# Performance work log

Hardware: AMD Instinct MI355X
Metric: run time of the kernel (lower is better)

The kernel has to match this reference:

```python
import jax, jax.numpy as jnp
import numpy as np

EPS = 1e-5


def setup_inputs() -> dict:
    key = jax.random.key(0)
    ks = jax.random.split(key, 7)
    BATCH, nbr, L, K, U = 64, 16, 64, 32, 4
    in1, in2, out = 64, 8, 32  # in2 = 2*U, out = K

    def unif(k, shape, fan_out, fan_in):
        ini = float(np.sqrt(3.0 / fan_out / fan_in))
        return jax.random.uniform(k, shape, jnp.float32, -ini, ini)

    return {
        "Hhat_real": jax.random.normal(ks[0], (BATCH, nbr, L, K, U), jnp.float32),
        "Hhat_imag": jax.random.normal(ks[1], (BATCH, nbr, L, K, U), jnp.float32),
        "Vhat": jax.random.normal(ks[2], (BATCH, nbr, L, K, U), jnp.float32),
        "Qs_hidden": unif(ks[3], (2, 4, in1, in1), in1, in1),  # Q1_AP,Q2_AP,Q1_UE,Q2_UE per hidden layer
        "Ps_hidden": unif(ks[4], (2, 2, in1, in2), in1, in2),  # P1_AP,P1_UE per hidden layer
        "Qs_out": unif(ks[5], (4, out, in1), out, in1),
        "Ps_out": unif(ks[6], (2, out, in2), out, in2),
        "bn_gamma": jnp.ones((2, in1), jnp.float32),
        "bn_beta": jnp.zeros((2, in1), jnp.float32),
        "nbrOfRealizations": nbr,
        "L": L,
        "K": K,
        "U": U,
    }


def _bn(x, gamma, beta):
    # BatchNorm1d in training mode: per-channel stats over (batch, spatial), biased variance
    m = x.mean(axis=(0, 2), keepdims=True)
    v = x.var(axis=(0, 2), keepdims=True)
    return (x - m) / jnp.sqrt(v + EPS) * gamma[None, :, None] + beta[None, :, None]


def _layer(A_AP, A_UE, H, Q1a, Q2a, Q1u, Q2u, P1a, P1u, gamma, beta, act):
    # A_AP: [B, in1, L], A_UE: [B, in1, K], H: [B, in2, L, K]
    new_AP = (2.0 * jnp.einsum('oi,bil->bol', Q1a, A_AP)
              + 2.0 * jnp.einsum('oi,bi->bo', Q2a, A_UE.mean(-1))[:, :, None]
              + 0.1 * jnp.einsum('oi,bil->bol', P1a, H.mean(-1)))
    new_UE = (2.0 * jnp.einsum('oi,bik->bok', Q1u, A_UE)
              + 2.0 * jnp.einsum('oi,bi->bo', Q2u, A_AP.mean(-1))[:, :, None]
              + 0.1 * jnp.einsum('oi,bik->bok', P1u, H.mean(-2)))
    if act:
        new_AP = jax.nn.relu(new_AP)
        new_UE = jax.nn.relu(new_UE)
    if gamma is not None:
        new_AP = _bn(new_AP, gamma, beta)
        new_UE = _bn(new_UE, gamma, beta)
    return new_AP, new_UE


def _forward(Hhat_real, Hhat_imag, Vhat, Qs_hidden, Ps_hidden, Qs_out, Ps_out,
             bn_gamma, bn_beta, nbr, L, K, U):
    BATCH = Hhat_real.shape[0]
    B = BATCH * nbr
    in1 = Qs_hidden.shape[-1]
    # [B,1,L,K,U] -> transpose(2,3) -> transpose(2,4) == permute (0,1,4,2,3)
    Hr = jnp.transpose(Hhat_real.reshape(B, 1, L, K, U), (0, 1, 4, 2, 3))
    Hi = jnp.transpose(Hhat_imag.reshape(B, 1, L, K, U), (0, 1, 4, 2, 3))
    H = jnp.concatenate([Hr, Hi], axis=1).reshape(B, 2 * U, L, K)  # [B, 2U, L, K]

    A_AP = jnp.zeros((B, in1, L), H.dtype)
    A_UE = jnp.zeros((B, in1, K), H.dtype)
    n_hidden = Qs_hidden.shape[0]
    for i in range(n_hidden):
        A_AP, A_UE = _layer(A_AP, A_UE, H,
                            Qs_hidden[i, 0], Qs_hidden[i, 1], Qs_hidden[i, 2], Qs_hidden[i, 3],
                            Ps_hidden[i, 0], Ps_hidden[i, 1],
                            bn_gamma[i], bn_beta[i], act=True)
    V_AP_out, _ = _layer(A_AP, A_UE, H,
                         Qs_out[0], Qs_out[1], Qs_out[2], Qs_out[3],
                         Ps_out[0], Ps_out[1], None, None, act=False)  # [B, K, L]

    Phat1 = jnp.swapaxes(V_AP_out.reshape(BATCH, nbr, K, L), 2, 3)  # [BATCH, nbr, L, K]
    norm = jnp.linalg.norm(Phat1, axis=2, keepdims=True)            # [BATCH, nbr, 1, K]
    Phat = Phat1 / norm * np.sqrt(float(L))
    Fhat = Vhat.reshape(BATCH, nbr, L, K, U) * Phat[..., None]
    return Fhat


def reference(Hhat_real, Hhat_imag, Vhat, Qs_hidden, Ps_hidden, Qs_out, Ps_out,
              bn_gamma, bn_beta, nbrOfRealizations, L, K, U):
    return _forward(Hhat_real, Hhat_imag, Vhat, Qs_hidden, Ps_hidden, Qs_out, Ps_out,
                    bn_gamma, bn_beta, int(nbrOfRealizations), int(L), int(K), int(U))
```

## Files before the change

kernel.cpp:

```cpp
#include <hip/hip_runtime.h>

#define B_TOT 1024
#define L_DIM 64
#define K_DIM 32
#define OUT_K 32
#define EPS_BN 1e-5f

typedef __attribute__((ext_vector_type(8))) short short8;
typedef __attribute__((ext_vector_type(4))) float f32x4;

__device__ __forceinline__ float reduce64(float v) {
    #pragma unroll
    for (int w = 1; w < 64; w <<= 1) v += __shfl_xor(v, w);
    return v;
}

template<int CTRL, int RM>
__device__ __forceinline__ float dppadd(float v) {
    return v + __int_as_float(__builtin_amdgcn_update_dpp(
        0, __float_as_int(v), CTRL, RM, 0xF, true));
}
__device__ __forceinline__ float sum64_dpp(float v) {
    v = dppadd<0x111, 0xF>(v);
    v = dppadd<0x112, 0xF>(v);
    v = dppadd<0x114, 0xF>(v);
    v = dppadd<0x118, 0xF>(v);
    v = dppadd<0x142, 0xA>(v);
    v = dppadd<0x143, 0xC>(v);
    return v;
}
__device__ __forceinline__ float sum32_dpp(float v) {
    v = dppadd<0x111, 0xF>(v);
    v = dppadd<0x112, 0xF>(v);
    v = dppadd<0x114, 0xF>(v);
    v = dppadd<0x118, 0xF>(v);
    v = dppadd<0x142, 0xA>(v);
    return v;
}

__device__ __forceinline__ unsigned short f2bf(float x) {
    unsigned int u = __float_as_uint(x);
    u += 0x7FFF + ((u >> 16) & 1);
    return (unsigned short)(u >> 16);
}

__global__ __launch_bounds__(256, 4) void hmeans_l0_kernel(
    const float* __restrict__ Hr, const float* __restrict__ Hi,
    float* __restrict__ Hmk, float* __restrict__ Hml,
    const float* __restrict__ P0,
    float* __restrict__ muS, float* __restrict__ muQ,
    const float* __restrict__ Qh1,
    const float* __restrict__ P1h,
    const float* __restrict__ Qo,
    float* __restrict__ QTo,
    unsigned short* __restrict__ Qpack_ap,
    unsigned short* __restrict__ Qpack_ue) {
    int b = blockIdx.x, tid = threadIdx.x;

    if (b == B_TOT) {
        for (int idx = tid; idx < 2048; idx += 256) {
            int i = idx >> 5, o = idx & 31;
            QTo[idx] = Qo[o * 64 + i];
        }
        const float* Q1a = Qh1;
        const float* Q1u = Qh1 + 2 * 4096;
        const float* P1a = P1h;
        const float* P1u = P1h + 512;
        for (int idx = tid; idx < 6144; idx += 256) {
            int j = idx & 7, lane = (idx >> 3) & 63, ot = (idx >> 9) & 3, kt = idx >> 11;
            int m = lane & 15, kloc = (lane >> 4) * 8 + j;
            int o = ot * 16 + m, k = kt * 32 + kloc;
            float va = 0.f, vu = 0.f;
            if (k < 64)      { va = 2.0f * Q1a[o * 64 + k]; vu = 2.0f * Q1u[o * 64 + k]; }
            else if (k < 72) { va = 0.1f * P1a[o * 8 + (k - 64)]; vu = 0.1f * P1u[o * 8 + (k - 64)]; }
            Qpack_ap[idx] = f2bf(va);
            Qpack_ue[idx] = f2bf(vu);
        }
        return;
    }

    __shared__ float hmkS[512];
    __shared__ float hmlS[256];
    __shared__ float4 wpart[4][32];
    int w = tid >> 6, lane = tid & 63;
    int g = tid >> 5, k = tid & 31;

    for (int ri = 0; ri < 2; ++ri) {
        const float4* src4 = (const float4*)((ri ? Hi : Hr) + (size_t)b * 8192);
        float4 v[8];
        #pragma unroll
        for (int s = 0; s < 8; ++s) v[s] = src4[tid + 256 * s];

        float4 part = v[0];
        #pragma unroll
        for (int s = 1; s < 8; ++s) {
            part.x += v[s].x; part.y += v[s].y;
            part.z += v[s].z; part.w += v[s].w;
        }

        #pragma unroll
        for (int s = 0; s < 8; ++s) {
            float rx = sum32_dpp(v[s].x);
            float ry = sum32_dpp(v[s].y);
            float rz = sum32_dpp(v[s].z);
            float rw = sum32_dpp(v[s].w);
            if ((lane & 31) == 31) {
                int l = g + 8 * s;
                const float sc = 1.0f / 32.0f;
                hmkS[(ri * 4 + 0) * 64 + l] = rx * sc;
                hmkS[(ri * 4 + 1) * 64 + l] = ry * sc;
                hmkS[(ri * 4 + 2) * 64 + l] = rz * sc;
                hmkS[(ri * 4 + 3) * 64 + l] = rw * sc;
            }
        }

        part.x += __shfl_xor(part.x, 32);
        part.y += __shfl_xor(part.y, 32);
        part.z += __shfl_xor(part.z, 32);
        part.w += __shfl_xor(part.w, 32);
        if (lane < 32) wpart[w][k] = part;
        __syncthreads();
        if (tid < 128) {
            int kk = tid >> 2, u = tid & 3;
            float s = ((const float*)&wpart[0][kk])[u]
                    + ((const float*)&wpart[1][kk])[u]
                    + ((const float*)&wpart[2][kk])[u]
                    + ((const float*)&wpart[3][kk])[u];
            hmlS[(ri * 4 + u) * 32 + kk] = s * (1.0f / 64.0f);
        }
        __syncthreads();
    }

    Hmk[(size_t)b * 512 + tid]       = hmkS[tid];
    Hmk[(size_t)b * 512 + 256 + tid] = hmkS[256 + tid];
    Hml[(size_t)b * 256 + tid]       = hmlS[tid];

    int o0 = __builtin_amdgcn_readfirstlane(w << 4);
    float hmk[8], hml[8];
    #pragma unroll
    for (int c = 0; c < 8; ++c) hmk[c] = hmkS[c * 64 + lane];
    #pragma unroll
    for (int c = 0; c < 8; ++c) hml[c] = hmlS[c * 32 + (lane & 31)];

    for (int h = 0; h < 2; ++h) {
        float vs[8], qs[8];
        #pragma unroll
        for (int mm = 0; mm < 8; ++mm) {
            int o = o0 + h * 8 + mm;
            float4 p0 = *(const float4*)(P0 + o * 8);
            float4 p1 = *(const float4*)(P0 + o * 8 + 4);
            float pa = p0.x * hmk[0] + p0.y * hmk[1] + p0.z * hmk[2] + p0.w * hmk[3]
                     + p1.x * hmk[4] + p1.y * hmk[5] + p1.z * hmk[6] + p1.w * hmk[7];
            float v = fmaxf(0.1f * pa, 0.f);
            vs[mm] = sum64_dpp(v);
            qs[mm] = sum64_dpp(v * v);
        }
        if (lane == 63) {
            #pragma unroll
            for (int mm = 0; mm < 8; ++mm) {
                muS[b * 128 + o0 + h * 8 + mm] = vs[mm];
                muQ[b * 128 + o0 + h * 8 + mm] = qs[mm];
            }
        }
    }
    for (int h = 0; h < 2; ++h) {
        float vs[8], qs[8];
        #pragma unroll
        for (int mm = 0; mm < 8; ++mm) {
            int o = o0 + h * 8 + mm;
            float4 p0 = *(const float4*)(P0 + 512 + o * 8);
            float4 p1 = *(const float4*)(P0 + 512 + o * 8 + 4);
            float pu = p0.x * hml[0] + p0.y * hml[1] + p0.z * hml[2] + p0.w * hml[3]
                     + p1.x * hml[4] + p1.y * hml[5] + p1.z * hml[6] + p1.w * hml[7];
            float v = fmaxf(0.1f * pu, 0.f);
            vs[mm] = sum64_dpp(v);
            qs[mm] = sum64_dpp(v * v);
        }
        if (lane == 63) {
            #pragma unroll
            for (int mm = 0; mm < 8; ++mm) {
                muS[b * 128 + 64 + o0 + h * 8 + mm] = vs[mm] * 0.5f;
                muQ[b * 128 + 64 + o0 + h * 8 + mm] = qs[mm] * 0.5f;
            }
        }
    }
}

__global__ __launch_bounds__(256, 2) void layer_hidden1_kernel(
    float* __restrict__ Aap_out,
    const float* __restrict__ Hmk, const float* __restrict__ Hml,
    const unsigned short* __restrict__ Qpack_ap,
    const unsigned short* __restrict__ Qpack_ue,
    const float* __restrict__ P0,
    const float* __restrict__ coefA,
    const float* __restrict__ biasIn,
    float* __restrict__ muS, float* __restrict__ muQ) {
    __shared__ unsigned short Bap[64 * 104];
    __shared__ unsigned short Bue[32 * 104];
    int b = blockIdx.x, t = threadIdx.x;

    {
        int l = t & 63, wid = t >> 6, i0 = wid << 4;
        float hmk[8];
        #pragma unroll
        for (int c = 0; c < 8; ++c) hmk[c] = Hmk[(size_t)b * 512 + c * 64 + l];
        unsigned short tmp[16];
        #pragma unroll
        for (int m = 0; m < 16; ++m) {
            int i = i0 + m;
            float4 p0 = *(const float4*)(P0 + i * 8);
            float4 p1 = *(const float4*)(P0 + i * 8 + 4);
            float pa = p0.x * hmk[0] + p0.y * hmk[1] + p0.z * hmk[2] + p0.w * hmk[3]
                     + p1.x * hmk[4] + p1.y * hmk[5] + p1.z * hmk[6] + p1.w * hmk[7];
            float a0 = fmaxf(0.1f * pa, 0.f);
            tmp[m] = f2bf(a0 * coefA[i] + coefA[64 + i]);
        }
        short8 s0, s1;
        #pragma unroll
        for (int j = 0; j < 8; ++j) { s0[j] = (short)tmp[j]; s1[j] = (short)tmp[8 + j]; }
        *(short8*)(&Bap[l * 104 + i0]) = s0;
        *(short8*)(&Bap[l * 104 + i0 + 8]) = s1;
        if (wid == 0) {
            #pragma unroll
            for (int c = 0; c < 8; ++c) Bap[l * 104 + 64 + c] = f2bf(hmk[c]);
            #pragma unroll
            for (int c = 72; c < 96; ++c) Bap[l * 104 + c] = 0;
        }
    }
    {
        int k = t & 31, g = t >> 5, i0 = g << 3;
        float hml[8];
        #pragma unroll
        for (int c = 0; c < 8; ++c) hml[c] = Hml[(size_t)b * 256 + c * 32 + k];
        unsigned short tu[8];
        #pragma unroll
        for (int m = 0; m < 8; ++m) {
            int i = i0 + m;
            float4 p0 = *(const float4*)(P0 + 512 + i * 8);
            float4 p1 = *(const float4*)(P0 + 512 + i * 8 + 4);
            float pu = p0.x * hml[0] + p0.y * hml[1] + p0.z * hml[2] + p0.w * hml[3]
                     + p1.x * hml[4] + p1.y * hml[5] + p1.z * hml[6] + p1.w * hml[7];
            float a0 = fmaxf(0.1f * pu, 0.f);
            tu[m] = f2bf(a0 * coefA[128 + i] + coefA[192 + i]);
        }
        short8 s0;
        #pragma unroll
        for (int j = 0; j < 8; ++j) s0[j] = (short)tu[j];
        *(short8*)(&Bue[k * 104 + i0]) = s0;
        if (t < 32) {
            #pragma unroll
            for (int c = 0; c < 8; ++c) Bue[k * 104 + 64 + c] = f2bf(hml[c]);
            #pragma unroll
            for (int c = 72; c < 96; ++c) Bue[k * 104 + c] = 0;
        }
    }
    __syncthreads();

    int lane = t & 63, w = t >> 6;
    int m16 = lane & 15, g4 = lane >> 4;
    int obase = w * 16 + g4 * 4;

    short8 aq[3], aqu[3];
    #pragma unroll
    for (int kt = 0; kt < 3; ++kt) {
        aq[kt]  = *(const short8*)(Qpack_ap + (((kt * 4 + w) * 64 + lane) << 3));
        aqu[kt] = *(const short8*)(Qpack_ue + (((kt * 4 + w) * 64 + lane) << 3));
    }

    float vsum[4] = {0.f, 0.f, 0.f, 0.f}, vsq[4] = {0.f, 0.f, 0.f, 0.f};
    #pragma unroll
    for (int lt = 0; lt < 4; ++lt) {
        f32x4 acc = *(const f32x4*)(biasIn + b * 128 + obase);
        #pragma unroll
        for (int kt = 0; kt < 3; ++kt) {
            short8 bf = *(const short8*)(&Bap[(lt * 16 + m16) * 104 + kt * 32 + g4 * 8]);
            acc = __builtin_amdgcn_mfma_f32_16x16x32_bf16(aq[kt], bf, acc, 0, 0, 0);
        }
        int lsp = lt * 16 + m16;
        #pragma unroll
        for (int r = 0; r < 4; ++r) {
            float v = fmaxf(acc[r], 0.f);
            Aap_out[(size_t)b * 4096 + (obase + r) * 64 + lsp] = v;
            vsum[r] += v; vsq[r] += v * v;
        }
    }
    #pragma unroll
    for (int s = 1; s < 16; s <<= 1) {
        #pragma unroll
        for (int r = 0; r < 4; ++r) {
            vsum[r] += __shfl_xor(vsum[r], s);
            vsq[r]  += __shfl_xor(vsq[r], s);
        }
    }
    if (m16 == 0) {
        #pragma unroll
        for (int r = 0; r < 4; ++r) {
            muS[b * 128 + obase + r] = vsum[r];
            muQ[b * 128 + obase + r] = vsq[r];
        }
    }

    float usum[4] = {0.f, 0.f, 0.f, 0.f}, usq[4] = {0.f, 0.f, 0.f, 0.f};
    #pragma unroll
    for (int nt = 0; nt < 2; ++nt) {
        f32x4 acc = *(const f32x4*)(biasIn + b * 128 + 64 + obase);
        #pragma unroll
        for (int kt = 0; kt < 3; ++kt) {
            short8 bf = *(const short8*)(&Bue[(nt * 16 + m16) * 104 + kt * 32 + g4 * 8]);
            acc = __builtin_amdgcn_mfma_f32_16x16x32_bf16(aqu[kt], bf, acc, 0, 0, 0);
        }
        #pragma unroll
        for (int r = 0; r < 4; ++r) {
            float v = fmaxf(acc[r], 0.f);
            usum[r] += v; usq[r] += v * v;
        }
    }
    #pragma unroll
    for (int s = 1; s < 16; s <<= 1) {
        #pragma unroll
        for (int r = 0; r < 4; ++r) {
            usum[r] += __shfl_xor(usum[r], s);
            usq[r]  += __shfl_xor(usq[r], s);
        }
    }
    if (m16 == 0) {
        #pragma unroll
        for (int r = 0; r < 4; ++r) {
            muS[b * 128 + 64 + obase + r] = usum[r];
            muQ[b * 128 + 64 + obase + r] = usq[r];
        }
    }
}

__global__ __launch_bounds__(256, 8) void bn_finalize_kernel(
    const float* __restrict__ muS, const float* __restrict__ muQ,
    const float* __restrict__ gamma, const float* __restrict__ beta,
    float* __restrict__ coef) {
    __shared__ float redS[4], redQ[4];
    int ch = blockIdx.x;
    int tid = threadIdx.x;
    float s = 0.f, q = 0.f;
    for (int j = tid; j < 1024; j += 256) {
        s += muS[j * 128 + ch];
        q += muQ[j * 128 + ch];
    }
    s = reduce64(s);
    q = reduce64(q);
    int wave = tid >> 6, lane = tid & 63;
    if (lane == 0) { redS[wave] = s; redQ[wave] = q; }
    __syncthreads();
    if (tid == 0) {
        s = redS[0] + redS[1] + redS[2] + redS[3];
        q = redQ[0] + redQ[1] + redQ[2] + redQ[3];
        bool ap = ch < 64;
        int o = ap ? ch : ch - 64;
        float cnt = ap ? (float)(B_TOT * L_DIM) : (float)(B_TOT * K_DIM);
        float m = s / cnt;
        float var = q / cnt - m * m;
        float sc = gamma[o] / sqrtf(var + EPS_BN);
        if (ap) { coef[o] = sc;       coef[64 + o] = beta[o] - m * sc; }
        else    { coef[128 + o] = sc; coef[192 + o] = beta[o] - m * sc; }
    }
}

__global__ __launch_bounds__(128, 8) void bias_hidden_kernel(
    const float* __restrict__ Q, const float* __restrict__ coef,
    const float* __restrict__ muS, float* __restrict__ bias) {
    __shared__ float mubn[128];
    int b = blockIdx.x, t = threadIdx.x;
    float raw = muS[b * 128 + t];
    if (t < 64) mubn[t] = raw * (1.0f / 64.0f) * coef[t] + coef[64 + t];
    else        mubn[t] = raw * (1.0f / 32.0f) * coef[64 + t] + coef[128 + t];
    __syncthreads();
    const float* Qm = (t < 64) ? (Q + 4096) : (Q + 3 * 4096);
    const float* mu = (t < 64) ? (mubn + 64) : mubn;
    int o = t & 63;
    const float4* Qrow = (const float4*)(Qm + o * 64);
    float sa = 0.f, sb = 0.f, sc2 = 0.f, sd = 0.f;
    #pragma unroll
    for (int j = 0; j < 16; ++j) {
        float4 q = Qrow[j];
        sa += q.x * mu[4 * j];
        sb += q.y * mu[4 * j + 1];
        sc2 += q.z * mu[4 * j + 2];
        sd += q.w * mu[4 * j + 3];
    }
    bias[b * 128 + t] = 2.f * ((sa + sb) + (sc2 + sd));
}

__global__ __launch_bounds__(64, 8) void bias_out_kernel(
    const float* __restrict__ Qo, const float* __restrict__ coef,
    const float* __restrict__ muS, float* __restrict__ biasO) {
    __shared__ float mubn[64];
    int b = blockIdx.x, t = threadIdx.x;
    mubn[t] = muS[b * 128 + 64 + t] * (1.0f / 32.0f) * coef[128 + t] + coef[192 + t];
    __syncthreads();
    if (t < 32) {
        const float4* Qrow = (const float4*)(Qo + OUT_K * 64 + t * 64);
        float sa = 0.f, sb = 0.f, sc2 = 0.f, sd = 0.f;
        #pragma unroll
        for (int j = 0; j < 16; ++j) {
            float4 q = Qrow[j];
            sa += q.x * mubn[4 * j];
            sb += q.y * mubn[4 * j + 1];
            sc2 += q.z * mubn[4 * j + 2];
            sd += q.w * mubn[4 * j + 3];
        }
        biasO[b * 32 + t] = 2.f * ((sa + sb) + (sc2 + sd));
    }
}

__global__ __launch_bounds__(256, 4) void layer_out_fin_kernel(
    const float* __restrict__ Aap_in,
    const float* __restrict__ Hmk,
    const float* __restrict__ QTo,
    const float* __restrict__ Po,
    const float* __restrict__ coefIn,
    const float* __restrict__ biasO,
    const float* __restrict__ Vhat,
    float* __restrict__ out) {
    __shared__ float sV[32 * 65];
    __shared__ float inv[32];
    int b = blockIdx.x, tid = threadIdx.x;
    int wid = tid >> 6, lane = tid & 63;
    int ob = __builtin_amdgcn_readfirstlane(wid << 3);

    float hmk[8];
    #pragma unroll
    for (int c = 0; c < 8; ++c) hmk[c] = Hmk[(size_t)b * 512 + c * 64 + lane];

    float bp[8];
    #pragma unroll
    for (int m = 0; m < 8; ++m) {
        int o = ob + m;
        float4 p0 = *(const float4*)(Po + o * 8);
        float4 p1 = *(const float4*)(Po + o * 8 + 4);
        float pa = p0.x * hmk[0] + p0.y * hmk[1] + p0.z * hmk[2] + p0.w * hmk[3]
                 + p1.x * hmk[4] + p1.y * hmk[5] + p1.z * hmk[6] + p1.w * hmk[7];
        bp[m] = 0.1f * pa + biasO[b * 32 + o];
    }

    float acc[8];
    #pragma unroll
    for (int m = 0; m < 8; ++m) acc[m] = 0.f;
    {
        const float* A_in = Aap_in + (size_t)b * 4096 + lane;
        #pragma unroll 4
        for (int i = 0; i < 64; ++i) {
            float x = A_in[i * 64];
            float aa = x * coefIn[i] + coefIn[64 + i];
            float4 q0 = *(const float4*)(QTo + i * 32 + ob);
            float4 q1 = *(const float4*)(QTo + i * 32 + ob + 4);
            acc[0] += q0.x * aa; acc[1] += q0.y * aa;
            acc[2] += q0.z * aa; acc[3] += q0.w * aa;
            acc[4] += q1.x * aa; acc[5] += q1.y * aa;
            acc[6] += q1.z * aa; acc[7] += q1.w * aa;
        }
    }
    #pragma unroll
    for (int m = 0; m < 8; ++m)
        sV[(ob + m) * 65 + lane] = 2.f * acc[m] + bp[m];

    __syncthreads();
    if (tid < 32) {
        float s = 0.f;
        #pragma unroll
        for (int l = 0; l < 64; ++l) { float x = sV[tid * 65 + l]; s += x * x; }
        inv[tid] = 8.0f / sqrtf(s);
    }
    __syncthreads();
    const float4* vh4 = (const float4*)(Vhat + (size_t)b * 8192);
    float4* o4 = (float4*)out + (size_t)b * 2048;
    for (int j = tid; j < 2048; j += 256) {
        int l = j >> 5, kk = j & 31;
        float p = sV[kk * 65 + l] * inv[kk];
        float4 x = vh4[j];
        x.x *= p; x.y *= p; x.z *= p; x.w *= p;
        o4[j] = x;
    }
}

extern "C" void kernel_launch(void* const* d_in, const int* in_sizes, int n_in,
                              void* d_out, int out_size, void* d_ws, size_t ws_size,
                              hipStream_t stream) {
    const float* Hr        = (const float*)d_in[0];
    const float* Hi        = (const float*)d_in[1];
    const float* Vhat      = (const float*)d_in[2];
    const float* Qs_hidden = (const float*)d_in[3];
    const float* Ps_hidden = (const float*)d_in[4];
    const float* Qs_out    = (const float*)d_in[5];
    const float* Ps_out    = (const float*)d_in[6];
    const float* bn_gamma  = (const float*)d_in[7];
    const float* bn_beta   = (const float*)d_in[8];
    float* out = (float*)d_out;

    float* ws    = (float*)d_ws;
    float* Hmk   = ws;
    float* Hml   = Hmk + 524288;
    float* AapB  = Hml + 262144;
    float* muS   = AapB + 4194304;
    float* muQ   = muS + 131072;
    float* coefA = muQ + 131072;
    float* coefB = coefA + 256;
    float* biasA = coefB + 256;
    float* biasO = biasA + 131072;
    float* QTo   = biasO + 32768;
    unsigned short* Qpack_ap = (unsigned short*)(QTo + 2048);
    unsigned short* Qpack_ue = Qpack_ap + 6144;

    hipLaunchKernelGGL(hmeans_l0_kernel, dim3(B_TOT + 1), dim3(256), 0, stream,
                       Hr, Hi, Hmk, Hml, Ps_hidden, muS, muQ,
                       Qs_hidden + 4 * 4096, Ps_hidden + 2 * 512, Qs_out,
                       QTo, Qpack_ap, Qpack_ue);
    hipLaunchKernelGGL(bn_finalize_kernel, dim3(128), dim3(256), 0, stream,
                       muS, muQ, bn_gamma, bn_beta, coefA);
    hipLaunchKernelGGL(bias_hidden_kernel, dim3(B_TOT), dim3(128), 0, stream,
                       Qs_hidden + 4 * 4096, coefA, muS, biasA);

    hipLaunchKernelGGL(layer_hidden1_kernel, dim3(B_TOT), dim3(256), 0, stream,
                       AapB, Hmk, Hml, Qpack_ap, Qpack_ue,
                       Ps_hidden, coefA, biasA, muS, muQ);
    hipLaunchKernelGGL(bn_finalize_kernel, dim3(128), dim3(256), 0, stream,
                       muS, muQ, bn_gamma + 64, bn_beta + 64, coefB);
    hipLaunchKernelGGL(bias_out_kernel, dim3(B_TOT), dim3(64), 0, stream,
                       Qs_out, coefB, muS, biasO);

    hipLaunchKernelGGL(layer_out_fin_kernel, dim3(B_TOT), dim3(256), 0, stream,
                       AapB, Hmk, QTo, Ps_out, coefB, biasO, Vhat, out);
}
```

Before: 77.18 us.

## Recompute layer-1 activations in output kernel instead of storing to global

```diff
diff --git a/kernel.cpp b/kernel.cpp
--- a/kernel.cpp
+++ b/kernel.cpp
@@ -7,6 +7,7 @@
 #define EPS_BN 1e-5f
 
 typedef __attribute__((ext_vector_type(8))) short short8;
+typedef __attribute__((ext_vector_type(4))) short short4v;
 typedef __attribute__((ext_vector_type(4))) float f32x4;
 
 __device__ __forceinline__ float reduce64(float v) {
@@ -37,6 +38,13 @@
     v = dppadd<0x142, 0xA>(v);
     return v;
 }
+__device__ __forceinline__ float sum16_dpp(float v) {
+    v = dppadd<0x111, 0xF>(v);
+    v = dppadd<0x112, 0xF>(v);
+    v = dppadd<0x114, 0xF>(v);
+    v = dppadd<0x118, 0xF>(v);
+    return v;
+}
 
 __device__ __forceinline__ unsigned short f2bf(float x) {
     unsigned int u = __float_as_uint(x);
@@ -52,16 +60,13 @@
     const float* __restrict__ Qh1,
     const float* __restrict__ P1h,
     const float* __restrict__ Qo,
-    float* __restrict__ QTo,
+    const float* __restrict__ Po,
     unsigned short* __restrict__ Qpack_ap,
-    unsigned short* __restrict__ Qpack_ue) {
+    unsigned short* __restrict__ Qpack_ue,
+    unsigned short* __restrict__ Qpack_o) {
     int b = blockIdx.x, tid = threadIdx.x;
 
     if (b == B_TOT) {
-        for (int idx = tid; idx < 2048; idx += 256) {
-            int i = idx >> 5, o = idx & 31;
-            QTo[idx] = Qo[o * 64 + i];
-        }
         const float* Q1a = Qh1;
         const float* Q1u = Qh1 + 2 * 4096;
         const float* P1a = P1h;
@@ -76,6 +81,15 @@
             Qpack_ap[idx] = f2bf(va);
             Qpack_ue[idx] = f2bf(vu);
         }
+        for (int idx = tid; idx < 3072; idx += 256) {
+            int j = idx & 7, lane = (idx >> 3) & 63, ot = (idx >> 9) & 1, kt = idx >> 10;
+            int m = lane & 15, kloc = (lane >> 4) * 8 + j;
+            int o = ot * 16 + m, k = kt * 32 + kloc;
+            float v = 0.f;
+            if (k < 64)      v = 2.0f * Qo[o * 64 + k];
+            else if (k < 72) v = 0.1f * Po[o * 8 + (k - 64)];
+            Qpack_o[idx] = f2bf(v);
+        }
         return;
     }
 
@@ -186,17 +200,19 @@
     }
 }
 
-__global__ __launch_bounds__(256, 2) void layer_hidden1_kernel(
-    float* __restrict__ Aap_out,
+__global__ __launch_bounds__(256, 2) void l1stats_kernel(
     const float* __restrict__ Hmk, const float* __restrict__ Hml,
     const unsigned short* __restrict__ Qpack_ap,
     const unsigned short* __restrict__ Qpack_ue,
     const float* __restrict__ P0,
+    const float* __restrict__ Qh1,
     const float* __restrict__ coefA,
-    const float* __restrict__ biasIn,
-    float* __restrict__ muS, float* __restrict__ muQ) {
+    const float* __restrict__ muS0,
+    float* __restrict__ muS1, float* __restrict__ muQ1) {
     __shared__ unsigned short Bap[64 * 104];
     __shared__ unsigned short Bue[32 * 104];
+    __shared__ float mubn[128];
+    __shared__ float biasS[128];
     int b = blockIdx.x, t = threadIdx.x;
 
     {
@@ -254,6 +270,30 @@
             for (int c = 72; c < 96; ++c) Bue[k * 104 + c] = 0;
         }
     }
+    if (t < 128) {
+        float raw = muS0[b * 128 + t];
+        mubn[t] = (t < 64)
+            ? raw * (1.0f / 64.0f) * coefA[t] + coefA[64 + t]
+            : raw * (1.0f / 32.0f) * coefA[64 + t] + coefA[128 + t];
+    }
+    __syncthreads();
+
+    if (t < 128) {
+        const float* Qm = (t < 64) ? (Qh1 + 4096) : (Qh1 + 3 * 4096);
+        const float* mu = (t < 64) ? (mubn + 64) : mubn;
+        int o = t & 63;
+        const float4* Qrow = (const float4*)(Qm + o * 64);
+        float sa = 0.f, sb = 0.f, sc2 = 0.f, sd = 0.f;
+        #pragma unroll
+        for (int j = 0; j < 16; ++j) {
+            float4 q = Qrow[j];
+            sa += q.x * mu[4 * j];
+            sb += q.y * mu[4 * j + 1];
+            sc2 += q.z * mu[4 * j + 2];
+            sd += q.w * mu[4 * j + 3];
+        }
+        biasS[t] = 2.f * ((sa + sb) + (sc2 + sd));
+    }
     __syncthreads();
 
     int lane = t & 63, w = t >> 6;
@@ -270,40 +310,35 @@
     float vsum[4] = {0.f, 0.f, 0.f, 0.f}, vsq[4] = {0.f, 0.f, 0.f, 0.f};
     #pragma unroll
     for (int lt = 0; lt < 4; ++lt) {
-        f32x4 acc = *(const f32x4*)(biasIn + b * 128 + obase);
+        f32x4 acc = *(const f32x4*)(&biasS[obase]);
         #pragma unroll
         for (int kt = 0; kt < 3; ++kt) {
             short8 bf = *(const short8*)(&Bap[(lt * 16 + m16) * 104 + kt * 32 + g4 * 8]);
             acc = __builtin_amdgcn_mfma_f32_16x16x32_bf16(aq[kt], bf, acc, 0, 0, 0);
         }
-        int lsp = lt * 16 + m16;
         #pragma unroll
         for (int r = 0; r < 4; ++r) {
             float v = fmaxf(acc[r], 0.f);
-            Aap_out[(size_t)b * 4096 + (obase + r) * 64 + lsp] = v;
             vsum[r] += v; vsq[r] += v * v;
         }
     }
     #pragma unroll
-    for (int s = 1; s < 16; s <<= 1) {
+    for (int r = 0; r < 4; ++r) {
+        vsum[r] = sum16_dpp(vsum[r]);
+        vsq[r]  = sum16_dpp(vsq[r]);
+    }
+    if (m16 == 15) {
         #pragma unroll
         for (int r = 0; r < 4; ++r) {
-            vsum[r] += __shfl_xor(vsum[r], s);
-            vsq[r]  += __shfl_xor(vsq[r], s);
-        }
-    }
-    if (m16 == 0) {
-        #pragma unroll
-        for (int r = 0; r < 4; ++r) {
-            muS[b * 128 + obase + r] = vsum[r];
-            muQ[b * 128 + obase + r] = vsq[r];
+            muS1[b * 128 + obase + r] = vsum[r];
+            muQ1[b * 128 + obase + r] = vsq[r];
         }
     }
 
     float usum[4] = {0.f, 0.f, 0.f, 0.f}, usq[4] = {0.f, 0.f, 0.f, 0.f};
     #pragma unroll
     for (int nt = 0; nt < 2; ++nt) {
-        f32x4 acc = *(const f32x4*)(biasIn + b * 128 + 64 + obase);
+        f32x4 acc = *(const f32x4*)(&biasS[64 + obase]);
         #pragma unroll
         for (int kt = 0; kt < 3; ++kt) {
             short8 bf = *(const short8*)(&Bue[(nt * 16 + m16) * 104 + kt * 32 + g4 * 8]);
@@ -316,18 +351,15 @@
         }
     }
     #pragma unroll
-    for (int s = 1; s < 16; s <<= 1) {
+    for (int r = 0; r < 4; ++r) {
+        usum[r] = sum16_dpp(usum[r]);
+        usq[r]  = sum16_dpp(usq[r]);
+    }
+    if (m16 == 15) {
         #pragma unroll
         for (int r = 0; r < 4; ++r) {
-            usum[r] += __shfl_xor(usum[r], s);
-            usq[r]  += __shfl_xor(usq[r], s);
-        }
-    }
-    if (m16 == 0) {
-        #pragma unroll
-        for (int r = 0; r < 4; ++r) {
-            muS[b * 128 + 64 + obase + r] = usum[r];
-            muQ[b * 128 + 64 + obase + r] = usq[r];
+            muS1[b * 128 + 64 + obase + r] = usum[r];
+            muQ1[b * 128 + 64 + obase + r] = usq[r];
         }
     }
 }
@@ -363,115 +395,163 @@
     }
 }
 
-__global__ __launch_bounds__(128, 8) void bias_hidden_kernel(
-    const float* __restrict__ Q, const float* __restrict__ coef,
-    const float* __restrict__ muS, float* __restrict__ bias) {
-    __shared__ float mubn[128];
+__global__ __launch_bounds__(256, 2) void out_fin_kernel(
+    const float* __restrict__ Hmk,
+    const unsigned short* __restrict__ Qpack_ap,
+    const unsigned short* __restrict__ Qpack_o,
+    const float* __restrict__ P0,
+    const float* __restrict__ Qh1,
+    const float* __restrict__ Qo,
+    const float* __restrict__ coefA,
+    const float* __restrict__ coefB,
+    const float* __restrict__ muS0,
+    const float* __restrict__ muS1,
+    const float* __restrict__ Vhat,
+    float* __restrict__ out) {
+    __shared__ unsigned short Bap[64 * 104];
+    __shared__ unsigned short B2[64 * 104];
+    __shared__ float sV[32 * 65];
+    __shared__ float mubnA[64], mubnB[64];
+    __shared__ float biasA_S[64], biasO_S[32];
+    __shared__ float cB[128];
+    __shared__ float inv[32];
     int b = blockIdx.x, t = threadIdx.x;
-    float raw = muS[b * 128 + t];
-    if (t < 64) mubn[t] = raw * (1.0f / 64.0f) * coef[t] + coef[64 + t];
-    else        mubn[t] = raw * (1.0f / 32.0f) * coef[64 + t] + coef[128 + t];
-    __syncthreads();
-    const float* Qm = (t < 64) ? (Q + 4096) : (Q + 3 * 4096);
-    const float* mu = (t < 64) ? (mubn + 64) : mubn;
-    int o = t & 63;
-    const float4* Qrow = (const float4*)(Qm + o * 64);
-    float sa = 0.f, sb = 0.f, sc2 = 0.f, sd = 0.f;
-    #pragma unroll
-    for (int j = 0; j < 16; ++j) {
-        float4 q = Qrow[j];
-        sa += q.x * mu[4 * j];
-        sb += q.y * mu[4 * j + 1];
-        sc2 += q.z * mu[4 * j + 2];
-        sd += q.w * mu[4 * j + 3];
-    }
-    bias[b * 128 + t] = 2.f * ((sa + sb) + (sc2 + sd));
-}
-
-__global__ __launch_bounds__(64, 8) void bias_out_kernel(
-    const float* __restrict__ Qo, const float* __restrict__ coef,
-    const float* __restrict__ muS, float* __restrict__ biasO) {
-    __shared__ float mubn[64];
-    int b = blockIdx.x, t = threadIdx.x;
-    mubn[t] = muS[b * 128 + 64 + t] * (1.0f / 32.0f) * coef[128 + t] + coef[192 + t];
-    __syncthreads();
-    if (t < 32) {
-        const float4* Qrow = (const float4*)(Qo + OUT_K * 64 + t * 64);
+    int lane = t & 63, w = t >> 6;
+
+    {
+        int l = lane, i0 = w << 4;
+        float hmk[8];
+        #pragma unroll
+        for (int c = 0; c < 8; ++c) hmk[c] = Hmk[(size_t)b * 512 + c * 64 + l];
+        unsigned short tmp[16];
+        #pragma unroll
+        for (int m = 0; m < 16; ++m) {
+            int i = i0 + m;
+            float4 p0 = *(const float4*)(P0 + i * 8);
+            float4 p1 = *(const float4*)(P0 + i * 8 + 4);
+            float pa = p0.x * hmk[0] + p0.y * hmk[1] + p0.z * hmk[2] + p0.w * hmk[3]
+                     + p1.x * hmk[4] + p1.y * hmk[5] + p1.z * hmk[6] + p1.w * hmk[7];
+            float a0 = fmaxf(0.1f * pa, 0.f);
+            tmp[m] = f2bf(a0 * coefA[i] + coefA[64 + i]);
+        }
+        short8 s0, s1;
+        #pragma unroll
+        for (int j = 0; j < 8; ++j) { s0[j] = (short)tmp[j]; s1[j] = (short)tmp[8 + j]; }
+        *(short8*)(&Bap[l * 104 + i0]) = s0;
+        *(short8*)(&Bap[l * 104 + i0 + 8]) = s1;
+        if (w == 0) {
+            #pragma unroll
+            for (int c = 0; c < 8; ++c) {
+                unsigned short hb = f2bf(hmk[c]);
+                Bap[l * 104 + 64 + c] = hb;
+                B2[l * 104 + 64 + c]  = hb;
+            }
+            #pragma unroll
+            for (int c = 72; c < 96; ++c) { Bap[l * 104 + c] = 0; B2[l * 104 + c] = 0; }
+        }
+    }
+    if (t < 64)  mubnA[t] = muS0[b * 128 + 64 + t] * (1.0f / 32.0f) * coefA[128 + t] + coefA[192 + t];
+    else if (t < 128) {
+        int i = t - 64;
+        mubnB[i] = muS1[b * 128 + 64 + i] * (1.0f / 32.0f) * coefB[128 + i] + coefB[192 + i];
+    } else if (t < 256 && t >= 128) {
+        cB[t - 128] = coefB[t - 128];
+    }
+    __syncthreads();
+
+    if (t < 64) {
+        const float4* Qrow = (const float4*)(Qh1 + 4096 + t * 64);
         float sa = 0.f, sb = 0.f, sc2 = 0.f, sd = 0.f;
         #pragma unroll
         for (int j = 0; j < 16; ++j) {
             float4 q = Qrow[j];
-            sa += q.x * mubn[4 * j];
-            sb += q.y * mubn[4 * j + 1];
-            sc2 += q.z * mubn[4 * j + 2];
-            sd += q.w * mubn[4 * j + 3];
-        }
-        biasO[b * 32 + t] = 2.f * ((sa + sb) + (sc2 + sd));
-    }
-}
-
-__global__ __launch_bounds__(256, 4) void layer_out_fin_kernel(
-    const float* __restrict__ Aap_in,
-    const float* __restrict__ Hmk,
-    const float* __restrict__ QTo,
-    const float* __restrict__ Po,
-    const float* __restrict__ coefIn,
-    const float* __restrict__ biasO,
-    const float* __restrict__ Vhat,
-    float* __restrict__ out) {
-    __shared__ float sV[32 * 65];
-    __shared__ float inv[32];
-    int b = blockIdx.x, tid = threadIdx.x;
-    int wid = tid >> 6, lane = tid & 63;
-    int ob = __builtin_amdgcn_readfirstlane(wid << 3);
-
-    float hmk[8];
-    #pragma unroll
-    for (int c = 0; c < 8; ++c) hmk[c] = Hmk[(size_t)b * 512 + c * 64 + lane];
-
-    float bp[8];
-    #pragma unroll
-    for (int m = 0; m < 8; ++m) {
-        int o = ob + m;
-        float4 p0 = *(const float4*)(Po + o * 8);
-        float4 p1 = *(const float4*)(Po + o * 8 + 4);
-        float pa = p0.x * hmk[0] + p0.y * hmk[1] + p0.z * hmk[2] + p0.w * hmk[3]
-                 + p1.x * hmk[4] + p1.y * hmk[5] + p1.z * hmk[6] + p1.w * hmk[7];
-        bp[m] = 0.1f * pa + biasO[b * 32 + o];
-    }
-
-    float acc[8];
-    #pragma unroll
-    for (int m = 0; m < 8; ++m) acc[m] = 0.f;
+            sa += q.x * mubnA[4 * j];
+            sb += q.y * mubnA[4 * j + 1];
+            sc2 += q.z * mubnA[4 * j + 2];
+            sd += q.w * mubnA[4 * j + 3];
+        }
+        biasA_S[t] = 2.f * ((sa + sb) + (sc2 + sd));
+    } else if (t < 96) {
+        int o = t - 64;
+        const float4* Qrow = (const float4*)(Qo + OUT_K * 64 + o * 64);
+        float sa = 0.f, sb = 0.f, sc2 = 0.f, sd = 0.f;
+        #pragma unroll
+        for (int j = 0; j < 16; ++j) {
+            float4 q = Qrow[j];
+            sa += q.x * mubnB[4 * j];
+            sb += q.y * mubnB[4 * j + 1];
+            sc2 += q.z * mubnB[4 * j + 2];
+            sd += q.w * mubnB[4 * j + 3];
+        }
+        biasO_S[o] = 2.f * ((sa + sb) + (sc2 + sd));
+    }
+    __syncthreads();
+
+    int m16 = lane & 15, g4 = lane >> 4;
+    int obase = w * 16 + g4 * 4;
+
     {
-        const float* A_in = Aap_in + (size_t)b * 4096 + lane;
-        #pragma unroll 4
-        for (int i = 0; i < 64; ++i) {
-            float x = A_in[i * 64];
-            float aa = x * coefIn[i] + coefIn[64 + i];
-            float4 q0 = *(const float4*)(QTo + i * 32 + ob);
-            float4 q1 = *(const float4*)(QTo + i * 32 + ob + 4);
-            acc[0] += q0.x * aa; acc[1] += q0.y * aa;
-            acc[2] += q0.z * aa; acc[3] += q0.w * aa;
-            acc[4] += q1.x * aa; acc[5] += q1.y * aa;
-            acc[6] += q1.z * aa; acc[7] += q1.w * aa;
-        }
-    }
-    #pragma unroll
-    for (int m = 0; m < 8; ++m)
-        sV[(ob + m) * 65 + lane] = 2.f * acc[m] + bp[m];
-
-    __syncthreads();
-    if (tid < 32) {
+        short8 aq[3];
+        #pragma unroll
+        for (int kt = 0; kt < 3; ++kt)
+            aq[kt] = *(const short8*)(Qpack_ap + (((kt * 4 + w) * 64 + lane) << 3));
+        float scb[4], shb[4];
+        #pragma unroll
+        for (int r = 0; r < 4; ++r) { scb[r] = cB[obase + r]; shb[r] = cB[64 + obase + r]; }
+        #pragma unroll
+        for (int lt = 0; lt < 4; ++lt) {
+            f32x4 acc = *(const f32x4*)(&biasA_S[obase]);
+            #pragma unroll
+            for (int kt = 0; kt < 3; ++kt) {
+                short8 bf = *(const short8*)(&Bap[(lt * 16 + m16) * 104 + kt * 32 + g4 * 8]);
+                acc = __builtin_amdgcn_mfma_f32_16x16x32_bf16(aq[kt], bf, acc, 0, 0, 0);
+            }
+            int lsp = lt * 16 + m16;
+            short4v pk;
+            #pragma unroll
+            for (int r = 0; r < 4; ++r) {
+                float v = fmaxf(acc[r], 0.f);
+                pk[r] = (short)f2bf(v * scb[r] + shb[r]);
+            }
+            *(short4v*)(&B2[lsp * 104 + obase]) = pk;
+        }
+    }
+    __syncthreads();
+
+    {
+        int ot = w & 1;
+        short8 aq[3];
+        #pragma unroll
+        for (int kt = 0; kt < 3; ++kt)
+            aq[kt] = *(const short8*)(Qpack_o + (((kt * 2 + ot) * 64 + lane) << 3));
+        int ch0 = ot * 16 + g4 * 4;
+        #pragma unroll
+        for (int h = 0; h < 2; ++h) {
+            int lt = (w >> 1) + 2 * h;
+            f32x4 acc = *(const f32x4*)(&biasO_S[ch0]);
+            #pragma unroll
+            for (int kt = 0; kt < 3; ++kt) {
+                short8 bf = *(const short8*)(&B2[(lt * 16 + m16) * 104 + kt * 32 + g4 * 8]);
+                acc = __builtin_amdgcn_mfma_f32_16x16x32_bf16(aq[kt], bf, acc, 0, 0, 0);
+            }
+            int l = lt * 16 + m16;
+            #pragma unroll
+            for (int r = 0; r < 4; ++r)
+                sV[(ch0 + r) * 65 + l] = acc[r];
+        }
+    }
+    __syncthreads();
+
+    if (t < 32) {
         float s = 0.f;
         #pragma unroll
-        for (int l = 0; l < 64; ++l) { float x = sV[tid * 65 + l]; s += x * x; }
-        inv[tid] = 8.0f / sqrtf(s);
+        for (int l = 0; l < 64; ++l) { float x = sV[t * 65 + l]; s += x * x; }
+        inv[t] = 8.0f / sqrtf(s);
     }
     __syncthreads();
     const float4* vh4 = (const float4*)(Vhat + (size_t)b * 8192);
     float4* o4 = (float4*)out + (size_t)b * 2048;
-    for (int j = tid; j < 2048; j += 256) {
+    for (int j = t; j < 2048; j += 256) {
         int l = j >> 5, kk = j & 31;
         float p = sV[kk * 65 + l] * inv[kk];
         float4 x = vh4[j];
@@ -497,34 +577,29 @@
     float* ws    = (float*)d_ws;
     float* Hmk   = ws;
     float* Hml   = Hmk + 524288;
-    float* AapB  = Hml + 262144;
-    float* muS   = AapB + 4194304;
-    float* muQ   = muS + 131072;
-    float* coefA = muQ + 131072;
+    float* muS0  = Hml + 262144;
+    float* muQ0  = muS0 + 131072;
+    float* muS1  = muQ0 + 131072;
+    float* muQ1  = muS1 + 131072;
+    float* coefA = muQ1 + 131072;
     float* coefB = coefA + 256;
-    float* biasA = coefB + 256;
-    float* biasO = biasA + 131072;
-    float* QTo   = biasO + 32768;
-    unsigned short* Qpack_ap = (unsigned short*)(QTo + 2048);
+    unsigned short* Qpack_ap = (unsigned short*)(coefB + 256);
     unsigned short* Qpack_ue = Qpack_ap + 6144;
+    unsigned short* Qpack_o  = Qpack_ue + 6144;
 
     hipLaunchKernelGGL(hmeans_l0_kernel, dim3(B_TOT + 1), dim3(256), 0, stream,
-                       Hr, Hi, Hmk, Hml, Ps_hidden, muS, muQ,
-                       Qs_hidden + 4 * 4096, Ps_hidden + 2 * 512, Qs_out,
-                       QTo, Qpack_ap, Qpack_ue);
+                       Hr, Hi, Hmk, Hml, Ps_hidden, muS0, muQ0,
+                       Qs_hidden + 4 * 4096, Ps_hidden + 2 * 512, Qs_out, Ps_out,
+                       Qpack_ap, Qpack_ue, Qpack_o);
     hipLaunchKernelGGL(bn_finalize_kernel, dim3(128), dim3(256), 0, stream,
-                       muS, muQ, bn_gamma, bn_beta, coefA);
-    hipLaunchKernelGGL(bias_hidden_kernel, dim3(B_TOT), dim3(128), 0, stream,
-                       Qs_hidden + 4 * 4096, coefA, muS, biasA);
-
-    hipLaunchKernelGGL(layer_hidden1_kernel, dim3(B_TOT), dim3(256), 0, stream,
-                       AapB, Hmk, Hml, Qpack_ap, Qpack_ue,
-                       Ps_hidden, coefA, biasA, muS, muQ);
+                       muS0, muQ0, bn_gamma, bn_beta, coefA);
+    hipLaunchKernelGGL(l1stats_kernel, dim3(B_TOT), dim3(256), 0, stream,
+                       Hmk, Hml, Qpack_ap, Qpack_ue, Ps_hidden,
+                       Qs_hidden + 4 * 4096, coefA, muS0, muS1, muQ1);
     hipLaunchKernelGGL(bn_finalize_kernel, dim3(128), dim3(256), 0, stream,
-                       muS, muQ, bn_gamma + 64, bn_beta + 64, coefB);
-    hipLaunchKernelGGL(bias_out_kernel, dim3(B_TOT), dim3(64), 0, stream,
-                       Qs_out, coefB, muS, biasO);
-
-    hipLaunchKernelGGL(layer_out_fin_kernel, dim3(B_TOT), dim3(256), 0, stream,
-                       AapB, Hmk, QTo, Ps_out, coefB, biasO, Vhat, out);
-}
+                       muS1, muQ1, bn_gamma + 64, bn_beta + 64, coefB);
+    hipLaunchKernelGGL(out_fin_kernel, dim3(B_TOT), dim3(256), 0, stream,
+                       Hmk, Qpack_ap, Qpack_o, Ps_hidden,
+                       Qs_hidden + 4 * 4096, Qs_out, coefA, coefB,
+                       muS0, muS1, Vhat, out);
+}
```

Result: faster. 69.46 us (-10.0%).
